# Performance work log

Measured on AMD Instinct MI355X. Metric: run time of the kernel, lower is better.

The kernel has to match this reference:

```python
import jax, jax.numpy as jnp
import numpy as np

B, T, C = 8, 2048, 512
H = 8
DH = C // H
MLP = 4 * C
EPS = 1e-5


def _ln(x, w, b):
    m = jnp.mean(x, axis=-1, keepdims=True)
    v = jnp.mean(jnp.square(x - m), axis=-1, keepdims=True)
    return (x - m) * jax.lax.rsqrt(v + EPS) * w + b


def setup_inputs() -> dict:
    key = jax.random.key(0)
    ks = jax.random.split(key, 12)
    s = 0.02
    return {
        "x": jax.random.normal(ks[0], (B, T, C), jnp.float32),
        "c": jax.random.normal(ks[1], (B, C), jnp.float32),
        "qkv_w": jax.random.normal(ks[2], (3 * C, C), jnp.float32) * s,
        "qkv_b": jnp.zeros((3 * C,), jnp.float32),
        "proj_w": jax.random.normal(ks[3], (C, C), jnp.float32) * s,
        "proj_b": jnp.zeros((C,), jnp.float32),
        "ada_w": jax.random.normal(ks[4], (6 * C, C), jnp.float32) * s,
        "ada_b": jnp.zeros((6 * C,), jnp.float32),
        "fc1_w": jax.random.normal(ks[5], (MLP, C), jnp.float32) * s,
        "fc1_b": jnp.zeros((MLP,), jnp.float32),
        "fc2_w": jax.random.normal(ks[6], (C, MLP), jnp.float32) * s,
        "fc2_b": jnp.zeros((C,), jnp.float32),
        "ln1_w": jnp.ones((C,), jnp.float32),
        "ln1_b": jnp.zeros((C,), jnp.float32),
        "ln2_w": jnp.ones((C,), jnp.float32),
        "ln2_b": jnp.zeros((C,), jnp.float32),
    }


def reference(x, c, qkv_w, qkv_b, proj_w, proj_b, ada_w, ada_b,
              fc1_w, fc1_b, fc2_w, fc2_b, ln1_w, ln1_b, ln2_w, ln2_b):
    # AdaLN modulation: SiLU -> Linear -> chunk into 6 [B,C] pieces
    mod = jax.nn.silu(c) @ ada_w.T + ada_b  # [B, 6C]
    sh_msa, sc_msa, g_msa, sh_mlp, sc_mlp, g_mlp = jnp.split(mod, 6, axis=1)

    # --- attention branch ---
    h = _ln(x, ln1_w, ln1_b) * (1.0 + sc_msa[:, None, :]) + sh_msa[:, None, :]
    qkv = h @ qkv_w.T + qkv_b  # [B, T, 3C]
    q, k, v = jnp.split(qkv, 3, axis=-1)
    q = q.reshape(B, T, H, DH).transpose(0, 2, 1, 3)  # [B,H,T,Dh]
    k = k.reshape(B, T, H, DH).transpose(0, 2, 1, 3)
    v = v.reshape(B, T, H, DH).transpose(0, 2, 1, 3)
    scores = jnp.einsum('bhqd,bhkd->bhqk', q, k) * (1.0 / np.sqrt(DH))
    w = jax.nn.softmax(scores, axis=-1)
    o = jnp.einsum('bhqk,bhkd->bhqd', w, v)  # [B,H,T,Dh]
    o = o.transpose(0, 2, 1, 3).reshape(B, T, C)
    attn = o @ proj_w.T + proj_b
    x = x + g_msa[:, None, :] * attn

    # --- MLP branch ---
    h2 = _ln(x, ln2_w, ln2_b) * (1.0 + sc_mlp[:, None, :]) + sh_mlp[:, None, :]
    m = jax.nn.gelu(h2 @ fc1_w.T + fc1_b, approximate=True) @ fc2_w.T + fc2_b
    return x + g_mlp[:, None, :] * m
```

## Files before the change

### kernel.cpp

```cpp
#include <hip/hip_runtime.h>
#include <cstdint>
#include <cstddef>

typedef unsigned short u16;
typedef short v8s __attribute__((ext_vector_type(8)));
typedef float v4f __attribute__((ext_vector_type(4)));
typedef float f32x16 __attribute__((ext_vector_type(16)));
typedef unsigned int v4u __attribute__((ext_vector_type(4)));
typedef unsigned short v4u16 __attribute__((ext_vector_type(4)));

#define TT 2048
#define CC 512

#define QSCALE 0.18033688011112042f

__device__ __forceinline__ u16 f2bf(float f) {
    unsigned u = __float_as_uint(f);
    u += 0x7fffu + ((u >> 16) & 1u);
    return (u16)(u >> 16);
}

__device__ __forceinline__ float bf2f(u16 v) {
    return __uint_as_float(((unsigned)v) << 16);
}

__device__ __forceinline__ unsigned cvt_pk_bf16(float lo, float hi) {
    unsigned r;
    asm("v_cvt_pk_bf16_f32 %0, %1, %2" : "=v"(r) : "v"(lo), "v"(hi));
    return r;
}

__device__ __forceinline__ float fexp2(float x) {
    float xf = __builtin_floorf(x);
    float f = x - xf;
    float p = __builtin_fmaf(f,
              __builtin_fmaf(f,
              __builtin_fmaf(f, 0.0781455737f, 0.2261731467f),
                                0.6955568569f), 1.0f);
    int e = (int)xf;
    return __uint_as_float(__float_as_uint(p) + ((unsigned)(e << 23)));
}

__device__ __forceinline__ void swap32(unsigned a, unsigned b, unsigned& x, unsigned& y) {
#if __has_builtin(__builtin_amdgcn_permlane32_swap)
    auto r = __builtin_amdgcn_permlane32_swap(a, b, false, false);
    x = r[0]; y = r[1];
#else
    unsigned bx = (unsigned)__shfl_xor((int)b, 32, 64);
    unsigned ax = (unsigned)__shfl_xor((int)a, 32, 64);
    bool hi5 = (threadIdx.x & 32) != 0;
    x = hi5 ? bx : a;
    y = hi5 ? b : ax;
#endif
}

__device__ __forceinline__ void gl2lds16(const void* g, void* l) {
    __builtin_amdgcn_global_load_lds(
        (const __attribute__((address_space(1))) unsigned int*)g,
        (__attribute__((address_space(3))) unsigned int*)l,
        16, 0, 0);
}

__global__ __launch_bounds__(256) void f2bf_k(const float* __restrict__ s,
                                              u16* __restrict__ d, int n) {
    int i = (blockIdx.x * 256 + threadIdx.x) * 4;
    if (i >= n) return;
    float4 v = *(const float4*)(s + i);
    v4u16 r;
    r[0] = f2bf(v.x); r[1] = f2bf(v.y); r[2] = f2bf(v.z); r[3] = f2bf(v.w);
    *(v4u16*)(d + i) = r;
}

__global__ __launch_bounds__(256) void ada_kernel(const float* __restrict__ c,
                                                  const float* __restrict__ W,
                                                  const float* __restrict__ bias,
                                                  float* __restrict__ mod) {
    int idx = blockIdx.x * 4 + (threadIdx.x >> 6);
    int l = threadIdx.x & 63;
    int bb = idx / 3072;
    int n = idx - bb * 3072;
    const float* cp = c + bb * CC;
    const float* wp = W + (size_t)n * CC;
    float s = 0.f;
    #pragma unroll
    for (int i = 0; i < 8; ++i) {
        int k = l * 8 + i;
        float cv = cp[k];
        float sil = cv / (1.f + __expf(-cv));
        s += sil * wp[k];
    }
    #pragma unroll
    for (int off = 32; off; off >>= 1) s += __shfl_xor(s, off, 64);
    if (l == 0) mod[idx] = s + bias[n];
}

__global__ __launch_bounds__(256) void ln_mod_kernel(const float* __restrict__ X,
                                                     const float* __restrict__ lnw,
                                                     const float* __restrict__ lnb,
                                                     const float* __restrict__ mod,
                                                     int sh_off, int sc_off,
                                                     u16* __restrict__ out) {
    int row = blockIdx.x * 4 + (threadIdx.x >> 6);
    int l = threadIdx.x & 63;
    int b = row >> 11;
    const float* xr = X + (size_t)row * CC + l * 8;
    float4 va = *(const float4*)(xr);
    float4 vb = *(const float4*)(xr + 4);
    float v[8] = {va.x, va.y, va.z, va.w, vb.x, vb.y, vb.z, vb.w};
    float s = 0.f;
    #pragma unroll
    for (int i = 0; i < 8; ++i) s += v[i];
    #pragma unroll
    for (int off = 32; off; off >>= 1) s += __shfl_xor(s, off, 64);
    float mean = s * (1.f / CC);
    float q = 0.f;
    #pragma unroll
    for (int i = 0; i < 8; ++i) { float d = v[i] - mean; q += d * d; }
    #pragma unroll
    for (int off = 32; off; off >>= 1) q += __shfl_xor(q, off, 64);
    float rstd = rsqrtf(q * (1.f / CC) + 1e-5f);
    int col = l * 8;
    const float* shp = mod + b * 3072 + sh_off + col;
    const float* scp = mod + b * 3072 + sc_off + col;
    v8s st;
    #pragma unroll
    for (int i = 0; i < 8; ++i) {
        float hv = (v[i] - mean) * rstd * lnw[col + i] + lnb[col + i];
        float r = hv * (1.f + scp[i]) + shp[i];
        st[i] = (short)f2bf(r);
    }
    *(v8s*)(out + (size_t)row * CC + col) = st;
}

__global__ __launch_bounds__(512) void vt_kernel(const u16* __restrict__ qkv,
                                                 u16* __restrict__ vT) {
    __shared__ u16 tile[64 * 72];
    const int id = blockIdx.x;
    const int bh = id >> 5, tt = id & 31;
    const int b = bh >> 3, h = bh & 7;
    const int tid = threadIdx.x;
    const int tr = tid >> 3, d0 = (tid & 7) * 8;
    v8s v = *(const v8s*)(qkv + (size_t)(b * TT + tt * 64 + tr) * 1536 + 1024 + h * 64 + d0);
    *(v8s*)(&tile[tr * 72 + d0]) = v;
    __syncthreads();
    const int dr = tid >> 3, t0 = (tid & 7) * 8;
    v8s ov;
    #pragma unroll
    for (int e = 0; e < 8; ++e) ov[e] = (short)tile[(t0 + e) * 72 + dr];
    *(v8s*)(vT + (size_t)(bh * 64 + dr) * TT + tt * 64 + t0) = ov;
}

template <int MODE>
__global__ __launch_bounds__(256)
void gemm_bt(const u16* __restrict__ A, const u16* __restrict__ W,
             const float* __restrict__ bias, void* __restrict__ outp,
             const float* __restrict__ resid, const float* __restrict__ gate,
             int NX, int N, int K) {
    __shared__ alignas(16) u16 Al[2][4096];
    __shared__ alignas(16) u16 Bl[2][4096];
    const int id = blockIdx.x;
    const int wg = (id & 7) * (gridDim.x >> 3) + (id >> 3);
    const int by = wg / NX, bx = wg - by * NX;
    const int bn = bx << 7, bm = by << 7;
    const int tid = threadIdx.x;
    const int w = tid >> 6, l = tid & 63;
    const int hi = l >> 4, lo = l & 15;
    const int wr = (w >> 1) << 6, wc = (w & 1) << 6;

    v4f acc[4][4] = {};

    const int srow = l >> 2;
    const int sp = l & 3;
    const int NT = K >> 5;

    auto stage = [&](int buf, int kt) {
        const int k0 = kt << 5;
        #pragma unroll
        for (int i = 0; i < 2; ++i) {
            const int c = w + (i << 2);
            const int row = (c << 4) + srow;
            const int lg = sp ^ ((row >> 1) & 3);
            gl2lds16(A + (size_t)(bm + row) * K + k0 + (lg << 3), &Al[buf][c << 9]);
            gl2lds16(W + (size_t)(bn + row) * K + k0 + (lg << 3), &Bl[buf][c << 9]);
        }
    };

    stage(0, 0);
    __syncthreads();
    int cur = 0;
    for (int t = 0; t < NT; ++t) {
        if (t + 1 < NT) stage(cur ^ 1, t + 1);
        const u16* Ab = Al[cur];
        const u16* Bb = Bl[cur];
        v8s aF[4], bF[4];
        #pragma unroll
        for (int mi = 0; mi < 4; ++mi) {
            int r = wr + (mi << 4) + lo;
            aF[mi] = *(const v8s*)(Ab + (r << 5) + ((hi ^ ((r >> 1) & 3)) << 3));
        }
        #pragma unroll
        for (int ni = 0; ni < 4; ++ni) {
            int r = wc + (ni << 4) + lo;
            bF[ni] = *(const v8s*)(Bb + (r << 5) + ((hi ^ ((r >> 1) & 3)) << 3));
        }
        #pragma unroll
        for (int mi = 0; mi < 4; ++mi)
            #pragma unroll
            for (int ni = 0; ni < 4; ++ni)
                acc[mi][ni] = __builtin_amdgcn_mfma_f32_16x16x32_bf16(
                    aF[mi], bF[ni], acc[mi][ni], 0, 0, 0);
        __syncthreads();
        cur ^= 1;
    }

    #pragma unroll
    for (int mi = 0; mi < 4; ++mi) {
        #pragma unroll
        for (int ni = 0; ni < 4; ++ni) {
            int col = bn + wc + (ni << 4) + lo;
            float bv = bias[col];
            #pragma unroll
            for (int j = 0; j < 4; ++j) {
                int row = bm + wr + (mi << 4) + hi * 4 + j;
                float v = acc[mi][ni][j] + bv;
                if constexpr (MODE == 0) {
                    float sc2 = (col < 512) ? QSCALE : 1.0f;
                    ((u16*)outp)[(size_t)row * N + col] = f2bf(v * sc2);
                } else if constexpr (MODE == 1) {
                    float u2 = 1.5957691216057308f * (v + 0.044715f * v * v * v);
                    float g = v / (1.f + __expf(-u2));
                    ((u16*)outp)[(size_t)row * N + col] = f2bf(g);
                } else {
                    float r = resid[(size_t)row * N + col];
                    float gt = gate[(row >> 11) * 3072 + col];
                    ((float*)outp)[(size_t)row * N + col] = r + gt * v;
                }
            }
        }
    }
}

__global__ __launch_bounds__(512, 4)
void attn_kernel(const u16* __restrict__ qkv, const u16* __restrict__ vT,
                 u16* __restrict__ Opart, float* __restrict__ lpart) {
    __shared__ alignas(16) u16 smem[18432];
    const int tid = threadIdx.x;
    const int w = tid >> 6, l = tid & 63;
    const int l31 = l & 31, l5 = l >> 5;
    const int id = blockIdx.x;
    const int bh = id & 63, b = bh >> 3, h = bh & 7;
    const int qs = id >> 6, qt = qs >> 1, sp = qs & 1;

    const int qrow = qt * 256 + w * 32 + l31;
    const u16* qp = qkv + (size_t)(b * TT + qrow) * 1536 + h * 64;
    v8s qf[4];
    #pragma unroll
    for (int ks = 0; ks < 4; ++ks) qf[ks] = *(const v8s*)(qp + ks * 16 + l5 * 8);

    const int r8 = l >> 3;
    const int kc = (l & 7) ^ r8 ^ w;
    const u16* kptr = qkv + (size_t)(b * TT + sp * 1024 + 8 * w + r8) * 1536 + 512 + h * 64 + kc * 8;
    const u16* vptr = vT + (size_t)(bh * 64 + 8 * w + r8) * TT + sp * 1024 + kc * 8;

    auto stageKV = [&](int it, int buf) {
        gl2lds16(kptr + (size_t)it * 64 * 1536, smem + buf * 4096 + w * 512);
        gl2lds16(vptr + it * 64, smem + 8192 + buf * 4096 + w * 512);
    };

    const char* sbase = (const char*)smem;
    int offs[8];
    #pragma unroll
    for (int t = 0; t < 2; ++t)
        #pragma unroll
        for (int ks = 0; ks < 4; ++ks) {
            int row = t * 32 + l31;
            int phys = ((ks << 1) + l5) ^ (row & 7) ^ ((row >> 3) & 7);
            offs[t * 4 + ks] = row * 128 + phys * 16;
        }

    v8s onesf;
    #pragma unroll
    for (int i = 0; i < 8; ++i) onesf[i] = (short)0x3F80;

    stageKV(0, 0);
    __syncthreads();

    f32x16 o[2] = {};
    f32x16 lacc = {};

    #pragma unroll 2
    for (int it = 0; it < 16; ++it) {
        const int cur = it & 1;
        if (it + 1 < 16) stageKV(it + 1, cur ^ 1);
        const int koff = cur * 8192;

        f32x16 st[2];
        st[0] = (f32x16)0.f; st[1] = (f32x16)0.f;
        __builtin_amdgcn_s_setprio(1);
        #pragma unroll
        for (int ks = 0; ks < 4; ++ks) {
            v8s k0 = *(const v8s*)(sbase + offs[ks] + koff);
            v8s k1 = *(const v8s*)(sbase + offs[4 + ks] + koff);
            st[0] = __builtin_amdgcn_mfma_f32_32x32x16_bf16(k0, qf[ks], st[0], 0, 0, 0);
            st[1] = __builtin_amdgcn_mfma_f32_32x32x16_bf16(k1, qf[ks], st[1], 0, 0, 0);
        }
        __builtin_amdgcn_s_setprio(0);

        #pragma unroll
        for (int t2 = 0; t2 < 2; ++t2)
            #pragma unroll
            for (int r = 0; r < 16; ++r)
                st[t2][r] = fexp2(st[t2][r]);

        __builtin_amdgcn_s_setprio(1);
        #pragma unroll
        for (int ks = 0; ks < 4; ++ks) {
            const int tt = ks >> 1, rb = (ks & 1) * 8;
            unsigned pkA = cvt_pk_bf16(st[tt][rb + 0], st[tt][rb + 1]);
            unsigned pkB = cvt_pk_bf16(st[tt][rb + 4], st[tt][rb + 5]);
            unsigned pkC = cvt_pk_bf16(st[tt][rb + 2], st[tt][rb + 3]);
            unsigned pkD = cvt_pk_bf16(st[tt][rb + 6], st[tt][rb + 7]);
            unsigned w0, w1, w2, w3;
            swap32(pkA, pkB, w0, w2);
            swap32(pkC, pkD, w1, w3);
            v4u pw; pw[0] = w0; pw[1] = w1; pw[2] = w2; pw[3] = w3;
            v8s pa = __builtin_bit_cast(v8s, pw);
            v8s vf0 = *(const v8s*)(sbase + offs[ks] + koff + 16384);
            v8s vf1 = *(const v8s*)(sbase + offs[4 + ks] + koff + 16384);
            o[0] = __builtin_amdgcn_mfma_f32_32x32x16_bf16(vf0, pa, o[0], 0, 0, 0);
            o[1] = __builtin_amdgcn_mfma_f32_32x32x16_bf16(vf1, pa, o[1], 0, 0, 0);
            lacc = __builtin_amdgcn_mfma_f32_32x32x16_bf16(onesf, pa, lacc, 0, 0, 0);
        }
        __builtin_amdgcn_s_setprio(0);
        __syncthreads();
    }

    if (l5 == 0)
        lpart[(size_t)(sp * 64 + bh) * TT + qt * 256 + w * 32 + l31] = lacc[0];
    char* outw = (char*)smem + w * 4608;
    #pragma unroll
    for (int t2 = 0; t2 < 2; ++t2)
        #pragma unroll
        for (int r = 0; r < 16; r += 2) {
            int dh = t2 * 32 + (r & 3) + ((r >> 2) << 3) + (l5 << 2);
            unsigned pk = cvt_pk_bf16(o[t2][r], o[t2][r + 1]);
            *(unsigned*)(outw + l31 * 144 + dh * 2) = pk;
        }
    __syncthreads();
    u16* Ob = Opart + (size_t)sp * 16384 * 512;
    #pragma unroll
    for (int i = 0; i < 4; ++i) {
        int idx = (i << 9) + tid;
        int qq = idx >> 3, cch = idx & 7;
        v8s vd = *(const v8s*)((char*)smem + (qq >> 5) * 4608 + (qq & 31) * 144 + cch * 16);
        *(v8s*)(Ob + (size_t)(b * TT + qt * 256 + qq) * 512 + h * 64 + cch * 8) = vd;
    }
}

__global__ __launch_bounds__(256) void combine_k(const u16* __restrict__ Opart,
                                                 const float* __restrict__ lpart,
                                                 u16* __restrict__ out) {
    int idx = blockIdx.x * 256 + threadIdx.x;
    int t = idx >> 6, c0 = (idx & 63) << 3;
    int bh = ((t >> 11) << 3) + (c0 >> 6);
    float l0 = lpart[(size_t)bh * TT + (t & 2047)];
    float l1 = lpart[(size_t)(64 + bh) * TT + (t & 2047)];
    float inv = 1.f / (l0 + l1);
    v8s a = *(const v8s*)(Opart + (size_t)idx * 8);
    v8s b2 = *(const v8s*)(Opart + (size_t)16384 * 512 + (size_t)idx * 8);
    v8s r;
    #pragma unroll
    for (int e = 0; e < 8; ++e)
        r[e] = (short)f2bf((bf2f((u16)a[e]) + bf2f((u16)b2[e])) * inv);
    *(v8s*)(out + (size_t)idx * 8) = r;
}

extern "C" void kernel_launch(void* const* d_in, const int* in_sizes, int n_in,
                              void* d_out, int out_size, void* d_ws, size_t ws_size,
                              hipStream_t stream) {
    const float* x = (const float*)d_in[0];
    const float* c = (const float*)d_in[1];
    const float* qkv_w = (const float*)d_in[2];
    const float* qkv_b = (const float*)d_in[3];
    const float* proj_w = (const float*)d_in[4];
    const float* proj_b = (const float*)d_in[5];
    const float* ada_w = (const float*)d_in[6];
    const float* ada_b = (const float*)d_in[7];
    const float* fc1_w = (const float*)d_in[8];
    const float* fc1_b = (const float*)d_in[9];
    const float* fc2_w = (const float*)d_in[10];
    const float* fc2_b = (const float*)d_in[11];
    const float* ln1_w = (const float*)d_in[12];
    const float* ln1_b = (const float*)d_in[13];
    const float* ln2_w = (const float*)d_in[14];
    const float* ln2_b = (const float*)d_in[15];

    char* p = (char*)d_ws;
    auto carve = [&](size_t bytes) -> char* {
        char* r = p;
        p += (bytes + 255) & ~(size_t)255;
        return r;
    };
    float* mod  = (float*)carve((size_t)8 * 3072 * 4);
    u16* hbuf   = (u16*)carve((size_t)16384 * 512 * 2);
    u16* qkvb   = (u16*)carve((size_t)16384 * 1536 * 2);
    u16* attno  = (u16*)carve((size_t)16384 * 512 * 2);
    float* x1   = (float*)carve((size_t)16384 * 512 * 4);
    u16* wq     = (u16*)carve((size_t)1536 * 512 * 2);
    u16* wpj    = (u16*)carve((size_t)512 * 512 * 2);
    u16* w1     = (u16*)carve((size_t)2048 * 512 * 2);
    u16* w2     = (u16*)carve((size_t)512 * 2048 * 2);
    u16* fc1g   = qkvb;
    u16* Opart  = (u16*)x1;
    u16* vT     = hbuf;
    float* lprt = (float*)wq;

    f2bf_k<<<(1536 * 512) / 1024, 256, 0, stream>>>(qkv_w, wq, 1536 * 512);
    f2bf_k<<<(512 * 512) / 1024, 256, 0, stream>>>(proj_w, wpj, 512 * 512);
    f2bf_k<<<(2048 * 512) / 1024, 256, 0, stream>>>(fc1_w, w1, 2048 * 512);
    f2bf_k<<<(512 * 2048) / 1024, 256, 0, stream>>>(fc2_w, w2, 512 * 2048);

    ada_kernel<<<24576 / 4, 256, 0, stream>>>(c, ada_w, ada_b, mod);

    ln_mod_kernel<<<16384 / 4, 256, 0, stream>>>(x, ln1_w, ln1_b, mod, 0, 512, hbuf);
    gemm_bt<0><<<12 * 128, 256, 0, stream>>>(hbuf, wq, qkv_b, qkvb,
                                             nullptr, nullptr, 12, 1536, 512);
    vt_kernel<<<64 * 32, 512, 0, stream>>>(qkvb, vT);
    attn_kernel<<<1024, 512, 0, stream>>>(qkvb, vT, Opart, lprt);
    combine_k<<<4096, 256, 0, stream>>>(Opart, lprt, attno);
    gemm_bt<2><<<4 * 128, 256, 0, stream>>>(attno, wpj, proj_b, x1,
                                            x, mod + 2 * 512, 4, 512, 512);

    ln_mod_kernel<<<16384 / 4, 256, 0, stream>>>(x1, ln2_w, ln2_b, mod, 3 * 512, 4 * 512, hbuf);
    gemm_bt<1><<<16 * 128, 256, 0, stream>>>(hbuf, w1, fc1_b, fc1g,
                                             nullptr, nullptr, 16, 2048, 512);
    gemm_bt<2><<<4 * 128, 256, 0, stream>>>(fc1g, w2, fc2_b, (float*)d_out,
                                            x1, mod + 5 * 512, 4, 512, 2048);
}
```

Before: 333.7 us.

## Drop split-KV attention, normalize in-kernel, merge weight conversions into one launch

The attention kernel no longer splits the key range in two. Each block now loops over all 2048 keys and divides by the row sum itself, which removes the partial-output buffers and the separate combine kernel. The software exp2 polynomial is replaced with the hardware exp2 builtin. The four weight fp32-to-bf16 conversion launches are merged into one kernel writing a contiguous buffer. The cost is that the attention grid halves from 1024 to 512 blocks, lowering parallelism and occupancy across the CUs.

```diff
diff --git a/kernel.cpp b/kernel.cpp
--- a/kernel.cpp
+++ b/kernel.cpp
@@ -20,25 +20,10 @@
     return (u16)(u >> 16);
 }
 
-__device__ __forceinline__ float bf2f(u16 v) {
-    return __uint_as_float(((unsigned)v) << 16);
-}
-
 __device__ __forceinline__ unsigned cvt_pk_bf16(float lo, float hi) {
     unsigned r;
     asm("v_cvt_pk_bf16_f32 %0, %1, %2" : "=v"(r) : "v"(lo), "v"(hi));
     return r;
-}
-
-__device__ __forceinline__ float fexp2(float x) {
-    float xf = __builtin_floorf(x);
-    float f = x - xf;
-    float p = __builtin_fmaf(f,
-              __builtin_fmaf(f,
-              __builtin_fmaf(f, 0.0781455737f, 0.2261731467f),
-                                0.6955568569f), 1.0f);
-    int e = (int)xf;
-    return __uint_as_float(__float_as_uint(p) + ((unsigned)(e << 23)));
 }
 
 __device__ __forceinline__ void swap32(unsigned a, unsigned b, unsigned& x, unsigned& y) {
@@ -61,11 +46,18 @@
         16, 0, 0);
 }
 
-__global__ __launch_bounds__(256) void f2bf_k(const float* __restrict__ s,
-                                              u16* __restrict__ d, int n) {
+__global__ __launch_bounds__(256) void f2bf_all(const float* __restrict__ s0,
+                                                const float* __restrict__ s1,
+                                                const float* __restrict__ s2,
+                                                const float* __restrict__ s3,
+                                                u16* __restrict__ d) {
     int i = (blockIdx.x * 256 + threadIdx.x) * 4;
-    if (i >= n) return;
-    float4 v = *(const float4*)(s + i);
+    const float* s; int off;
+    if (i < 786432)       { s = s0; off = 0; }
+    else if (i < 1048576) { s = s1; off = 786432; }
+    else if (i < 2097152) { s = s2; off = 1048576; }
+    else                  { s = s3; off = 2097152; }
+    float4 v = *(const float4*)(s + (i - off));
     v4u16 r;
     r[0] = f2bf(v.x); r[1] = f2bf(v.y); r[2] = f2bf(v.z); r[3] = f2bf(v.w);
     *(v4u16*)(d + i) = r;
@@ -242,14 +234,14 @@
 
 __global__ __launch_bounds__(512, 4)
 void attn_kernel(const u16* __restrict__ qkv, const u16* __restrict__ vT,
-                 u16* __restrict__ Opart, float* __restrict__ lpart) {
+                 u16* __restrict__ O) {
     __shared__ alignas(16) u16 smem[18432];
     const int tid = threadIdx.x;
     const int w = tid >> 6, l = tid & 63;
     const int l31 = l & 31, l5 = l >> 5;
     const int id = blockIdx.x;
     const int bh = id & 63, b = bh >> 3, h = bh & 7;
-    const int qs = id >> 6, qt = qs >> 1, sp = qs & 1;
+    const int qt = id >> 6;
 
     const int qrow = qt * 256 + w * 32 + l31;
     const u16* qp = qkv + (size_t)(b * TT + qrow) * 1536 + h * 64;
@@ -259,8 +251,8 @@
 
     const int r8 = l >> 3;
     const int kc = (l & 7) ^ r8 ^ w;
-    const u16* kptr = qkv + (size_t)(b * TT + sp * 1024 + 8 * w + r8) * 1536 + 512 + h * 64 + kc * 8;
-    const u16* vptr = vT + (size_t)(bh * 64 + 8 * w + r8) * TT + sp * 1024 + kc * 8;
+    const u16* kptr = qkv + (size_t)(b * TT + 8 * w + r8) * 1536 + 512 + h * 64 + kc * 8;
+    const u16* vptr = vT + (size_t)(bh * 64 + 8 * w + r8) * TT + kc * 8;
 
     auto stageKV = [&](int it, int buf) {
         gl2lds16(kptr + (size_t)it * 64 * 1536, smem + buf * 4096 + w * 512);
@@ -289,9 +281,9 @@
     f32x16 lacc = {};
 
     #pragma unroll 2
-    for (int it = 0; it < 16; ++it) {
+    for (int it = 0; it < 32; ++it) {
         const int cur = it & 1;
-        if (it + 1 < 16) stageKV(it + 1, cur ^ 1);
+        if (it + 1 < 32) stageKV(it + 1, cur ^ 1);
         const int koff = cur * 8192;
 
         f32x16 st[2];
@@ -310,7 +302,7 @@
         for (int t2 = 0; t2 < 2; ++t2)
             #pragma unroll
             for (int r = 0; r < 16; ++r)
-                st[t2][r] = fexp2(st[t2][r]);
+                st[t2][r] = __builtin_exp2f(st[t2][r]);
 
         __builtin_amdgcn_s_setprio(1);
         #pragma unroll
@@ -335,44 +327,24 @@
         __syncthreads();
     }
 
-    if (l5 == 0)
-        lpart[(size_t)(sp * 64 + bh) * TT + qt * 256 + w * 32 + l31] = lacc[0];
+    float inv = 1.f / lacc[0];
     char* outw = (char*)smem + w * 4608;
     #pragma unroll
     for (int t2 = 0; t2 < 2; ++t2)
         #pragma unroll
         for (int r = 0; r < 16; r += 2) {
             int dh = t2 * 32 + (r & 3) + ((r >> 2) << 3) + (l5 << 2);
-            unsigned pk = cvt_pk_bf16(o[t2][r], o[t2][r + 1]);
+            unsigned pk = cvt_pk_bf16(o[t2][r] * inv, o[t2][r + 1] * inv);
             *(unsigned*)(outw + l31 * 144 + dh * 2) = pk;
         }
     __syncthreads();
-    u16* Ob = Opart + (size_t)sp * 16384 * 512;
     #pragma unroll
     for (int i = 0; i < 4; ++i) {
         int idx = (i << 9) + tid;
         int qq = idx >> 3, cch = idx & 7;
         v8s vd = *(const v8s*)((char*)smem + (qq >> 5) * 4608 + (qq & 31) * 144 + cch * 16);
-        *(v8s*)(Ob + (size_t)(b * TT + qt * 256 + qq) * 512 + h * 64 + cch * 8) = vd;
-    }
-}
-
-__global__ __launch_bounds__(256) void combine_k(const u16* __restrict__ Opart,
-                                                 const float* __restrict__ lpart,
-                                                 u16* __restrict__ out) {
-    int idx = blockIdx.x * 256 + threadIdx.x;
-    int t = idx >> 6, c0 = (idx & 63) << 3;
-    int bh = ((t >> 11) << 3) + (c0 >> 6);
-    float l0 = lpart[(size_t)bh * TT + (t & 2047)];
-    float l1 = lpart[(size_t)(64 + bh) * TT + (t & 2047)];
-    float inv = 1.f / (l0 + l1);
-    v8s a = *(const v8s*)(Opart + (size_t)idx * 8);
-    v8s b2 = *(const v8s*)(Opart + (size_t)16384 * 512 + (size_t)idx * 8);
-    v8s r;
-    #pragma unroll
-    for (int e = 0; e < 8; ++e)
-        r[e] = (short)f2bf((bf2f((u16)a[e]) + bf2f((u16)b2[e])) * inv);
-    *(v8s*)(out + (size_t)idx * 8) = r;
+        *(v8s*)(O + (size_t)(b * TT + qt * 256 + qq) * 512 + h * 64 + cch * 8) = vd;
+    }
 }
 
 extern "C" void kernel_launch(void* const* d_in, const int* in_sizes, int n_in,
@@ -406,19 +378,15 @@
     u16* qkvb   = (u16*)carve((size_t)16384 * 1536 * 2);
     u16* attno  = (u16*)carve((size_t)16384 * 512 * 2);
     float* x1   = (float*)carve((size_t)16384 * 512 * 4);
-    u16* wq     = (u16*)carve((size_t)1536 * 512 * 2);
-    u16* wpj    = (u16*)carve((size_t)512 * 512 * 2);
-    u16* w1     = (u16*)carve((size_t)2048 * 512 * 2);
-    u16* w2     = (u16*)carve((size_t)512 * 2048 * 2);
-    u16* fc1g   = qkvb;
-    u16* Opart  = (u16*)x1;
-    u16* vT     = hbuf;
-    float* lprt = (float*)wq;
-
-    f2bf_k<<<(1536 * 512) / 1024, 256, 0, stream>>>(qkv_w, wq, 1536 * 512);
-    f2bf_k<<<(512 * 512) / 1024, 256, 0, stream>>>(proj_w, wpj, 512 * 512);
-    f2bf_k<<<(2048 * 512) / 1024, 256, 0, stream>>>(fc1_w, w1, 2048 * 512);
-    f2bf_k<<<(512 * 2048) / 1024, 256, 0, stream>>>(fc2_w, w2, 512 * 2048);
+    u16* wall   = (u16*)carve((size_t)3145728 * 2);
+    u16* wq  = wall;
+    u16* wpj = wall + 786432;
+    u16* w1  = wall + 1048576;
+    u16* w2  = wall + 2097152;
+    u16* fc1g = qkvb;
+    u16* vT   = hbuf;
+
+    f2bf_all<<<3072, 256, 0, stream>>>(qkv_w, proj_w, fc1_w, fc2_w, wall);
 
     ada_kernel<<<24576 / 4, 256, 0, stream>>>(c, ada_w, ada_b, mod);
 
@@ -426,8 +394,7 @@
     gemm_bt<0><<<12 * 128, 256, 0, stream>>>(hbuf, wq, qkv_b, qkvb,
                                              nullptr, nullptr, 12, 1536, 512);
     vt_kernel<<<64 * 32, 512, 0, stream>>>(qkvb, vT);
-    attn_kernel<<<1024, 512, 0, stream>>>(qkvb, vT, Opart, lprt);
-    combine_k<<<4096, 256, 0, stream>>>(Opart, lprt, attno);
+    attn_kernel<<<512, 512, 0, stream>>>(qkvb, vT, attno);
     gemm_bt<2><<<4 * 128, 256, 0, stream>>>(attno, wpj, proj_b, x1,
                                             x, mod + 2 * 512, 4, 512, 512);
 
```

New measurement: 321.7 us. 1.04x faster.
